# Kernel tuning notes

Hardware: AMD Instinct MI355X
Metric: run time of the kernel (lower is better)

## Reference

```python
import jax, jax.numpy as jnp
import numpy as np

D_MODEL, D_STATE, D_CONV, EXPAND = 1024, 16, 4, 2
D_INNER = EXPAND * D_MODEL          # 2048
DT_RANK = D_MODEL // 16             # 64
B, L = 2, 1024


def setup_inputs() -> dict:
    key = jax.random.key(0)
    ks = jax.random.split(key, 10)
    x = jax.random.normal(ks[0], (B, L, D_MODEL), dtype=jnp.float32)
    ln_w = jnp.ones((D_MODEL,), jnp.float32)
    ln_b = jnp.zeros((D_MODEL,), jnp.float32)
    in_proj_w = jax.random.normal(ks[1], (2 * D_INNER, D_MODEL), jnp.float32) * (D_MODEL ** -0.5)
    conv_w = jax.random.normal(ks[2], (D_INNER, 1, D_CONV), jnp.float32) * (D_CONV ** -0.5)
    conv_b = jnp.zeros((D_INNER,), jnp.float32)
    x_proj_w = jax.random.normal(ks[3], (DT_RANK + 2 * D_STATE, D_INNER), jnp.float32) * (D_INNER ** -0.5)
    dt_proj_w = jax.random.normal(ks[4], (D_INNER, DT_RANK), jnp.float32) * (DT_RANK ** -0.5)
    # dt bias: inverse-softplus of dt sampled log-uniform in [1e-3, 1e-1] (mamba init)
    dt = jnp.exp(jax.random.uniform(ks[5], (D_INNER,)) * (np.log(0.1) - np.log(1e-3)) + np.log(1e-3))
    dt_proj_b = dt + jnp.log(-jnp.expm1(-dt))
    # A_log: log of [1..d_state] repeated per channel (S4D-real init)
    A_log = jnp.log(jnp.broadcast_to(jnp.arange(1, D_STATE + 1, dtype=jnp.float32), (D_INNER, D_STATE)))
    D = jnp.ones((D_INNER,), jnp.float32)
    out_proj_w = jax.random.normal(ks[6], (D_MODEL, D_INNER), jnp.float32) * (D_INNER ** -0.5)
    return dict(x=x, ln_w=ln_w, ln_b=ln_b, in_proj_w=in_proj_w, conv_w=conv_w,
                conv_b=conv_b, x_proj_w=x_proj_w, dt_proj_w=dt_proj_w,
                dt_proj_b=dt_proj_b, A_log=A_log, D=D, out_proj_w=out_proj_w)


def _layernorm(x, w, b, eps=1e-5):
    mu = jnp.mean(x, axis=-1, keepdims=True)
    var = jnp.mean(jnp.square(x - mu), axis=-1, keepdims=True)
    return (x - mu) * jax.lax.rsqrt(var + eps) * w + b


def _mamba(h, in_proj_w, conv_w, conv_b, x_proj_w, dt_proj_w, dt_proj_b, A_log, D, out_proj_w):
    # h: (B, L, d_model)
    xz = jnp.einsum('bld,ed->ble', h, in_proj_w)          # (B,L,2*d_inner)
    x_in, z = jnp.split(xz, 2, axis=-1)                   # each (B,L,d_inner)
    # depthwise causal conv1d
    kernel = jnp.transpose(conv_w, (2, 1, 0))             # (d_conv, 1, d_inner) LIO
    x_conv = jax.lax.conv_general_dilated(
        x_in, kernel, window_strides=(1,), padding=[(D_CONV - 1, 0)],
        dimension_numbers=('NLC', 'LIO', 'NLC'), feature_group_count=D_INNER)
    x_conv = jax.nn.silu(x_conv + conv_b)                 # (B,L,d_inner)
    # input-dependent SSM parameters
    x_dbl = jnp.einsum('bld,ed->ble', x_conv, x_proj_w)   # (B,L,dt_rank+2*d_state)
    dt, B_ssm, C_ssm = jnp.split(x_dbl, [DT_RANK, DT_RANK + D_STATE], axis=-1)
    dt = jax.nn.softplus(jnp.einsum('blr,dr->bld', dt, dt_proj_w) + dt_proj_b)  # (B,L,d_inner)
    A = -jnp.exp(A_log)                                   # (d_inner, d_state)
    deltaA = jnp.exp(dt[..., None] * A)                   # (B,L,d_inner,d_state)
    deltaBu = dt[..., None] * B_ssm[:, :, None, :] * x_conv[..., None]
    # selective scan: h_t = deltaA_t * h_{t-1} + deltaBu_t (parallel associative scan over L)
    def combine(left, right):
        a_l, b_l = left
        a_r, b_r = right
        return a_l * a_r, b_l * a_r + b_r
    _, states = jax.lax.associative_scan(combine, (deltaA, deltaBu), axis=1)
    y = jnp.einsum('blds,bls->bld', states, C_ssm) + x_conv * D
    y = y * jax.nn.silu(z)
    return jnp.einsum('bld,ed->ble', y, out_proj_w)       # (B,L,d_model)


def reference(x, ln_w, ln_b, in_proj_w, conv_w, conv_b, x_proj_w, dt_proj_w,
              dt_proj_b, A_log, D, out_proj_w):
    h = _layernorm(x, ln_w, ln_b)
    return x + _mamba(h, in_proj_w, conv_w, conv_b, x_proj_w, dt_proj_w,
                      dt_proj_b, A_log, D, out_proj_w)
```

## Files before the change

kernel.cpp:

```cpp
#include <hip/hip_runtime.h>
#include <hip/hip_bf16.h>
#include <math.h>

#define DM   1024
#define DI   2048
#define DS   16
#define DTR  64
#define NB   2
#define LL   1024
#define MR   (NB*LL)
#define XDBL 96
#define NC   32
#define CL   32

typedef _Float16 half8  __attribute__((ext_vector_type(8)));
typedef _Float16 half4v __attribute__((ext_vector_type(4)));
typedef float    floatx4 __attribute__((ext_vector_type(4)));

__device__ __forceinline__ void gload_lds16(const void* g, void* l) {
  __builtin_amdgcn_global_load_lds(
      (const __attribute__((address_space(1))) void*)g,
      (__attribute__((address_space(3))) void*)l, 16, 0, 0);
}

__global__ __launch_bounds__(256) void front_kernel(
    const float* __restrict__ x, const float* __restrict__ ln_w,
    const float* __restrict__ ln_b,
    const float* __restrict__ w_in, const float* __restrict__ w_out,
    const float* __restrict__ w_xp, const float* __restrict__ w_dt,
    _Float16* __restrict__ h_h,
    _Float16* __restrict__ w_in_h, _Float16* __restrict__ w_out_h,
    _Float16* __restrict__ w_xp_h, _Float16* __restrict__ w_dt_h) {
  const int blk = blockIdx.x;
  if (blk < MR) {
    __shared__ float sA[4], sB[4];
    const float* xr = x + (size_t)blk * DM;
    float s = 0.f, ss = 0.f;
    for (int i = threadIdx.x; i < DM; i += 256) {
      float v = xr[i];
      s += v; ss += v * v;
    }
    for (int o = 32; o > 0; o >>= 1) {
      s  += __shfl_down(s, o, 64);
      ss += __shfl_down(ss, o, 64);
    }
    const int wid = threadIdx.x >> 6, lid = threadIdx.x & 63;
    if (lid == 0) { sA[wid] = s; sB[wid] = ss; }
    __syncthreads();
    if (threadIdx.x == 0) {
      float S = sA[0] + sA[1] + sA[2] + sA[3];
      float SS = sB[0] + sB[1] + sB[2] + sB[3];
      float mu = S / DM;
      sA[0] = mu;
      sB[0] = rsqrtf(SS / DM - mu * mu + 1e-5f);
    }
    __syncthreads();
    const float mu = sA[0], rs = sB[0];
    for (int i = threadIdx.x; i < DM; i += 256)
      h_h[(size_t)blk * DM + i] = (_Float16)((xr[i] - mu) * rs * ln_w[i] + ln_b[i]);
    return;
  }
  int i = (blk - MR) * 256 + threadIdx.x;
  const int N0 = 1048576, N1 = 524288, N2 = 49152, N3 = 32768;
  const float* s; _Float16* d; int off;
  if (i < N0)            { s = w_in;  d = w_in_h;  off = i; }
  else if (i < N0+N1)    { s = w_out; d = w_out_h; off = i - N0; }
  else if (i < N0+N1+N2) { s = w_xp;  d = w_xp_h;  off = i - N0 - N1; }
  else if (i < N0+N1+N2+N3) { s = w_dt; d = w_dt_h; off = i - N0 - N1 - N2; }
  else return;
  float4 v = ((const float4*)s)[off];
  half4v h = {(_Float16)v.x, (_Float16)v.y, (_Float16)v.z, (_Float16)v.w};
  ((half4v*)d)[off] = h;
}

template <int EPI, int TN>
__global__ __launch_bounds__(256) void gemm_mfma(
    const _Float16* __restrict__ A,
    const _Float16* __restrict__ W,
    void* __restrict__ Cv, void* __restrict__ C2v,
    const float* __restrict__ extra, int ldc,
    int M, int N, int K, int kchunk) {
  constexpr int NT = (TN + 31) / 32;
  constexpr int WSLOT = TN / 16;
  constexpr int LPS = 2 + (WSLOT >= 8 ? 2 : 1);
  __shared__ alignas(16) _Float16 As[4][128 * 32];
  __shared__ alignas(16) _Float16 Ws[4][TN * 32];
  const int t = threadIdx.x;
  const int wave = t >> 6, lane = t & 63;
  const int m0 = blockIdx.y * 128, n0 = blockIdx.x * TN;
  const int k_beg = blockIdx.z * kchunk;
  const int nk = kchunk / 32;
  const int wm = (wave >> 1) * 64, wn = (wave & 1) * (TN / 2);
  floatx4 acc[4][NT];
#pragma unroll
  for (int i = 0; i < 4; i++)
#pragma unroll
    for (int j = 0; j < NT; j++) acc[i][j] = {0.f, 0.f, 0.f, 0.f};

  const int fr = lane & 15;
  const int kc8 = lane >> 4;
  const int kp = (kc8 ^ ((fr >> 1) & 3)) * 8;

  auto stage = [&](int buf, int k0) {
    for (int sl = wave; sl < 8; sl += 4) {
      const int idx = sl * 64 + lane;
      const int row = idx >> 2;
      const int kc = (idx & 3) ^ ((row >> 1) & 3);
      gload_lds16(A + (size_t)(m0 + row) * K + k0 + kc * 8,
                  &As[buf][sl * 512]);
    }
    for (int sl = wave; sl < WSLOT; sl += 4) {
      const int idx = sl * 64 + lane;
      const int row = idx >> 2;
      const int kc = (idx & 3) ^ ((row >> 1) & 3);
      const int wrow = (n0 + row < N) ? row : 0;
      gload_lds16(W + (size_t)(n0 + wrow) * K + k0 + kc * 8,
                  &Ws[buf][sl * 512]);
    }
  };

  const int npre = nk < 3 ? nk : 3;
  for (int p = 0; p < npre; p++) stage(p, k_beg + p * 32);

  for (int ki = 0; ki < nk; ki++) {
    const int rem = nk - 1 - ki;
    if (rem >= 2)
      asm volatile("s_waitcnt vmcnt(%0)" :: "n"(2 * LPS) : "memory");
    else if (rem == 1)
      asm volatile("s_waitcnt vmcnt(%0)" :: "n"(LPS) : "memory");
    else
      asm volatile("s_waitcnt vmcnt(0)" ::: "memory");
    __builtin_amdgcn_s_barrier();
    const int cur = ki & 3;
    half8 af[4], wf[NT];
#pragma unroll
    for (int i = 0; i < 4; i++)
      af[i] = *(const half8*)&As[cur][(wm + i * 16 + fr) * 32 + kp];
#pragma unroll
    for (int j = 0; j < NT; j++)
      wf[j] = *(const half8*)&Ws[cur][(wn + j * 16 + fr) * 32 + kp];
    __builtin_amdgcn_s_setprio(1);
#pragma unroll
    for (int i = 0; i < 4; i++)
#pragma unroll
      for (int j = 0; j < NT; j++)
        acc[i][j] = __builtin_amdgcn_mfma_f32_16x16x32_f16(af[i], wf[j], acc[i][j], 0, 0, 0);
    __builtin_amdgcn_s_setprio(0);
    if (ki + 3 < nk) stage((ki + 3) & 3, k_beg + (ki + 3) * 32);
  }

  const int col = lane & 15, rowq = lane >> 4;
#pragma unroll
  for (int i = 0; i < 4; i++) {
#pragma unroll
    for (int j = 0; j < NT; j++) {
      const int n = n0 + wn + j * 16 + col;
      if (n < N) {
#pragma unroll
        for (int r = 0; r < 4; r++) {
          const int m = m0 + wm + i * 16 + rowq * 4 + r;
          float v = acc[i][j][r];
          if (EPI == 0) {
            if (n < DI) ((_Float16*)Cv )[(size_t)m * DI + n]      = (_Float16)v;
            else        ((_Float16*)C2v)[(size_t)m * DI + n - DI] = (_Float16)v;
          } else if (EPI == 4) {
            ((_Float16*)Cv)[((size_t)blockIdx.z * M + m) * ldc + n] = (_Float16)v;
          } else if (EPI == 5) {
            v += extra[n];
            v = (v > 20.f) ? v : __logf(1.f + __expf(v));
            ((_Float16*)Cv)[(size_t)m * ldc + n] = (_Float16)v;
          }
        }
      }
    }
  }
}

__global__ __launch_bounds__(256) void xproj_reduce(
    const _Float16* __restrict__ part,
    float* __restrict__ x_dbl, _Float16* __restrict__ dtr) {
  const int idx = blockIdx.x * 256 + threadIdx.x;
  const int m = idx / XDBL, c = idx - m * XDBL;
  float s = 0.f;
#pragma unroll
  for (int z = 0; z < 16; z++) s += (float)part[(size_t)z * (MR * XDBL) + idx];
  x_dbl[idx] = s;
  if (c < DTR) dtr[m * DTR + c] = (_Float16)s;
}

__global__ __launch_bounds__(256) void out_reduce(
    const float* __restrict__ x, const _Float16* __restrict__ part,
    float* __restrict__ out) {
  const int i = blockIdx.x * 256 + threadIdx.x;
  float4 a = ((const float4*)x)[i];
#pragma unroll
  for (int z = 0; z < 4; z++) {
    half4v p = ((const half4v*)(part + (size_t)z * MR * DM))[i];
    a.x += (float)p.x; a.y += (float)p.y; a.z += (float)p.z; a.w += (float)p.w;
  }
  ((float4*)out)[i] = a;
}

__global__ __launch_bounds__(256) void conv_silu_kernel(
    const _Float16* __restrict__ xin, const float* __restrict__ cw,
    const float* __restrict__ cb, _Float16* __restrict__ xc) {
  const int idx = blockIdx.x * 256 + threadIdx.x;
  const int d8 = idx & (DI / 8 - 1);
  const int ml = idx >> 8;
  const int l  = ml & (LL - 1);
  const int d0 = d8 * 8;
  half8 xr[4];
  const half8 zero = {0, 0, 0, 0, 0, 0, 0, 0};
#pragma unroll
  for (int k = 0; k < 4; k++) {
    const int lp = l - 3 + k;
    xr[k] = (lp >= 0) ? *(const half8*)&xin[(size_t)(ml - 3 + k) * DI + d0] : zero;
  }
  half8 o;
#pragma unroll
  for (int j = 0; j < 8; j++) {
    float acc = cb[d0 + j];
#pragma unroll
    for (int k = 0; k < 4; k++)
      acc += (float)xr[k][j] * cw[(d0 + j) * 4 + k];
    o[j] = (_Float16)(acc / (1.f + __expf(-acc)));
  }
  *(half8*)&xc[(size_t)ml * DI + d0] = o;
}

__device__ __forceinline__ bool load_a(const float* __restrict__ A_log, int d,
                                       float* a) {
  const float4* Ap = (const float4*)(A_log + (size_t)d * DS);
  bool fast = true;
#pragma unroll
  for (int i = 0; i < 4; i++) {
    float4 v = Ap[i];
    a[4 * i + 0] = -__expf(v.x); a[4 * i + 1] = -__expf(v.y);
    a[4 * i + 2] = -__expf(v.z); a[4 * i + 3] = -__expf(v.w);
  }
#pragma unroll
  for (int s = 0; s < DS; s++)
    fast = fast && (fabsf(a[s] + (float)(s + 1)) < 1e-4f);
  return fast;
}

__global__ __launch_bounds__(256) void scan_phase1(
    const _Float16* __restrict__ xc,
    const float* __restrict__ xdbl,
    const _Float16* __restrict__ dtm,
    const float* __restrict__ A_log,
    float* __restrict__ HE,
    float* __restrict__ SA) {
  __shared__ float Bs[CL][DS];
  const int bi = blockIdx.x;
  const int dblk = bi & 7;
  const int c = (bi >> 3) & (NC - 1);
  const int b = bi >> 8;
  const int t = threadIdx.x;
  const int d = dblk * 256 + t;
  const int mlbase = b * LL + c * CL;

  for (int i = t; i < CL * DS; i += 256) {
    int tt = i >> 4, s = i & 15;
    Bs[tt][s] = xdbl[(size_t)(mlbase + tt) * XDBL + DTR + s];
  }

  float a[DS];
  const bool fast = load_a(A_log, d, a);
  float h[DS];
#pragma unroll
  for (int s = 0; s < DS; s++) h[s] = 0.f;
  float S = 0.f;
  __syncthreads();

  if (fast) {
    for (int tt = 0; tt < CL; tt++) {
      const size_t ml = mlbase + tt;
      const float dtv = (float)dtm[ml * DI + d];
      const float u   = (float)xc[ml * DI + d];
      const float du  = dtv * u;
      S += dtv;
      const float r = __expf(-dtv);
      float P = 1.f;
#pragma unroll
      for (int s = 0; s < DS; s++) {
        P *= r;
        h[s] = P * h[s] + du * Bs[tt][s];
      }
    }
  } else {
    for (int tt = 0; tt < CL; tt++) {
      const size_t ml = mlbase + tt;
      const float dtv = (float)dtm[ml * DI + d];
      const float u   = (float)xc[ml * DI + d];
      const float du  = dtv * u;
      S += dtv;
#pragma unroll
      for (int s = 0; s < DS; s++)
        h[s] = __expf(dtv * a[s]) * h[s] + du * Bs[tt][s];
    }
  }
  const size_t base = ((size_t)(b * NC + c) * DS) * DI + d;
#pragma unroll
  for (int s = 0; s < DS; s++) HE[base + (size_t)s * DI] = h[s];
  SA[(size_t)(b * NC + c) * DI + d] = S;
}

__global__ __launch_bounds__(256) void scan_phase2(
    const float* __restrict__ A_log,
    const float* __restrict__ SA,
    float* __restrict__ HE) {
  const int idx = blockIdx.x * 256 + threadIdx.x;
  const int d = idx & (DI - 1);
  const int s = (idx >> 11) & (DS - 1);
  const int b = idx >> 15;
  const float a = -__expf(A_log[(size_t)d * DS + s]);
  float Hc = 0.f;
  for (int c = 0; c < NC; c++) {
    const size_t o = ((size_t)(b * NC + c) * DS + s) * DI + d;
    const float he = HE[o];
    const float P = __expf(a * SA[(size_t)(b * NC + c) * DI + d]);
    HE[o] = Hc;
    Hc = P * Hc + he;
  }
}

__global__ __launch_bounds__(256) void scan_phase3(
    const _Float16* __restrict__ xc,
    const float* __restrict__ xdbl,
    const _Float16* __restrict__ dtm,
    const _Float16* __restrict__ zbuf,
    const float* __restrict__ A_log,
    const float* __restrict__ Dvec,
    const float* __restrict__ HE,
    _Float16* __restrict__ y) {
  __shared__ float Bs[CL][DS];
  __shared__ float Cs[CL][DS];
  const int bi = blockIdx.x;
  const int dblk = bi & 7;
  const int c = (bi >> 3) & (NC - 1);
  const int b = bi >> 8;
  const int t = threadIdx.x;
  const int d = dblk * 256 + t;
  const int mlbase = b * LL + c * CL;

  for (int i = t; i < CL * DS; i += 256) {
    int tt = i >> 4, s = i & 15;
    const size_t ro = (size_t)(mlbase + tt) * XDBL + DTR + s;
    Bs[tt][s] = xdbl[ro];
    Cs[tt][s] = xdbl[ro + DS];
  }

  float a[DS];
  const bool fast = load_a(A_log, d, a);
  float h[DS];
  const size_t base = ((size_t)(b * NC + c) * DS) * DI + d;
#pragma unroll
  for (int s = 0; s < DS; s++) h[s] = HE[base + (size_t)s * DI];
  const float Dv = Dvec[d];
  __syncthreads();

  if (fast) {
    for (int tt = 0; tt < CL; tt++) {
      const size_t ml = mlbase + tt;
      const float dtv = (float)dtm[ml * DI + d];
      const float u   = (float)xc[ml * DI + d];
      const float du  = dtv * u;
      const float r = __expf(-dtv);
      float P = 1.f, p = 0.f;
#pragma unroll
      for (int s = 0; s < DS; s++) {
        P *= r;
        h[s] = P * h[s] + du * Bs[tt][s];
        p += h[s] * Cs[tt][s];
      }
      const float zv = (float)zbuf[ml * DI + d];
      const float sil = zv / (1.f + __expf(-zv));
      y[ml * DI + d] = (_Float16)((p + u * Dv) * sil);
    }
  } else {
    for (int tt = 0; tt < CL; tt++) {
      const size_t ml = mlbase + tt;
      const float dtv = (float)dtm[ml * DI + d];
      const float u   = (float)xc[ml * DI + d];
      const float du  = dtv * u;
      float p = 0.f;
#pragma unroll
      for (int s = 0; s < DS; s++) {
        h[s] = __expf(dtv * a[s]) * h[s] + du * Bs[tt][s];
        p += h[s] * Cs[tt][s];
      }
      const float zv = (float)zbuf[ml * DI + d];
      const float sil = zv / (1.f + __expf(-zv));
      y[ml * DI + d] = (_Float16)((p + u * Dv) * sil);
    }
  }
}

extern "C" void kernel_launch(void* const* d_in, const int* in_sizes, int n_in,
                              void* d_out, int out_size, void* d_ws, size_t ws_size,
                              hipStream_t stream) {
  const float* x         = (const float*)d_in[0];
  const float* ln_w      = (const float*)d_in[1];
  const float* ln_b      = (const float*)d_in[2];
  const float* in_proj_w = (const float*)d_in[3];
  const float* conv_w    = (const float*)d_in[4];
  const float* conv_b    = (const float*)d_in[5];
  const float* x_proj_w  = (const float*)d_in[6];
  const float* dt_proj_w = (const float*)d_in[7];
  const float* dt_proj_b = (const float*)d_in[8];
  const float* A_log     = (const float*)d_in[9];
  const float* Dvec      = (const float*)d_in[10];
  const float* out_proj_w= (const float*)d_in[11];
  float* out = (float*)d_out;

  char* ws = (char*)d_ws;
  _Float16* h_h      = (_Float16*)ws;
  _Float16* xin_h    = (_Float16*)(ws + 4194304);
  _Float16* y_h      = xin_h;
  _Float16* z_h      = (_Float16*)(ws + 12582912);
  _Float16* xc_h     = (_Float16*)(ws + 20971520);
  _Float16* dtb_h    = (_Float16*)(ws + 29360128);
  _Float16* out_part = dtb_h;
  float*    x_dbl    = (float*)   (ws + 46137344);
  float*    SA       = (float*)   (ws + 46923776);
  _Float16* dtr_h    = (_Float16*)(ws + 47448064);
  float*    HE       = (float*)   (ws + 47710208);
  _Float16* w_in_h   = (_Float16*)(ws + 56098816);
  _Float16* w_out_h  = (_Float16*)(ws + 64487424);
  _Float16* w_xp_h   = (_Float16*)(ws + 68681728);
  _Float16* w_dt_h   = (_Float16*)(ws + 69074944);
  _Float16* xp_part  = (_Float16*)(ws + 69337088);

  front_kernel<<<MR + 6464, 256, 0, stream>>>(
      x, ln_w, ln_b, in_proj_w, out_proj_w, x_proj_w, dt_proj_w,
      h_h, w_in_h, w_out_h, w_xp_h, w_dt_h);

  gemm_mfma<0, 128><<<dim3(2 * DI / 128, MR / 128, 1), 256, 0, stream>>>(
      h_h, w_in_h, xin_h, z_h, nullptr, 0, MR, 2 * DI, DM, DM);

  conv_silu_kernel<<<(MR * DI / 8) / 256, 256, 0, stream>>>(xin_h, conv_w, conv_b, xc_h);

  gemm_mfma<4, 96><<<dim3(1, MR / 128, 16), 256, 0, stream>>>(
      xc_h, w_xp_h, xp_part, nullptr, nullptr, XDBL, MR, XDBL, DI, DI / 16);
  xproj_reduce<<<(MR * XDBL) / 256, 256, 0, stream>>>(xp_part, x_dbl, dtr_h);

  gemm_mfma<5, 64><<<dim3(DI / 64, MR / 128, 1), 256, 0, stream>>>(
      dtr_h, w_dt_h, dtb_h, nullptr, dt_proj_b, DI, MR, DI, DTR, DTR);

  scan_phase1<<<NB * NC * (DI / 256), 256, 0, stream>>>(
      xc_h, x_dbl, dtb_h, A_log, HE, SA);
  scan_phase2<<<(NB * DS * DI) / 256, 256, 0, stream>>>(A_log, SA, HE);
  scan_phase3<<<NB * NC * (DI / 256), 256, 0, stream>>>(
      xc_h, x_dbl, dtb_h, z_h, A_log, Dvec, HE, y_h);

  gemm_mfma<4, 128><<<dim3(DM / 128, MR / 128, 4), 256, 0, stream>>>(
      y_h, w_out_h, out_part, nullptr, nullptr, DM, MR, DM, DI, DI / 4);
  out_reduce<<<(MR * DM / 4) / 256, 256, 0, stream>>>(x, out_part, out);
}
```

Measured before the change: 224.8 us.

## Replace split-K partial buffers with atomic accumulation and fuse dt projection input conversion

The x_proj and out_proj split-K GEMMs now accumulate straight into fp32 outputs with atomicAdd. This removes the xproj_reduce and out_reduce kernels and their partial buffers. The residual is seeded by having the layernorm kernel copy x into out, and x_dbl is zeroed inside the conv kernel. A dedicated dt_kernel converts x_dbl to fp16 on the fly and applies bias plus softplus. Scan chunking also changes from 32 chunks of 32 to 16 chunks of 64. Atomics add contention and make the summation order nondeterministic.

```diff
diff --git a/kernel.cpp b/kernel.cpp
--- a/kernel.cpp
+++ b/kernel.cpp
@@ -10,8 +10,8 @@
 #define LL   1024
 #define MR   (NB*LL)
 #define XDBL 96
-#define NC   32
-#define CL   32
+#define NC   16
+#define CL   64
 
 typedef _Float16 half8  __attribute__((ext_vector_type(8)));
 typedef _Float16 half4v __attribute__((ext_vector_type(4)));
@@ -28,7 +28,7 @@
     const float* __restrict__ ln_b,
     const float* __restrict__ w_in, const float* __restrict__ w_out,
     const float* __restrict__ w_xp, const float* __restrict__ w_dt,
-    _Float16* __restrict__ h_h,
+    _Float16* __restrict__ h_h, float* __restrict__ out,
     _Float16* __restrict__ w_in_h, _Float16* __restrict__ w_out_h,
     _Float16* __restrict__ w_xp_h, _Float16* __restrict__ w_dt_h) {
   const int blk = blockIdx.x;
@@ -56,8 +56,11 @@
     }
     __syncthreads();
     const float mu = sA[0], rs = sB[0];
-    for (int i = threadIdx.x; i < DM; i += 256)
-      h_h[(size_t)blk * DM + i] = (_Float16)((xr[i] - mu) * rs * ln_w[i] + ln_b[i]);
+    for (int i = threadIdx.x; i < DM; i += 256) {
+      const float v = xr[i];
+      out[(size_t)blk * DM + i] = v;
+      h_h[(size_t)blk * DM + i] = (_Float16)((v - mu) * rs * ln_w[i] + ln_b[i]);
+    }
     return;
   }
   int i = (blk - MR) * 256 + threadIdx.x;
@@ -77,14 +80,13 @@
 __global__ __launch_bounds__(256) void gemm_mfma(
     const _Float16* __restrict__ A,
     const _Float16* __restrict__ W,
-    void* __restrict__ Cv, void* __restrict__ C2v,
-    const float* __restrict__ extra, int ldc,
+    void* __restrict__ Cv, void* __restrict__ C2v, int ldc,
     int M, int N, int K, int kchunk) {
   constexpr int NT = (TN + 31) / 32;
   constexpr int WSLOT = TN / 16;
   constexpr int LPS = 2 + (WSLOT >= 8 ? 2 : 1);
-  __shared__ alignas(16) _Float16 As[4][128 * 32];
-  __shared__ alignas(16) _Float16 Ws[4][TN * 32];
+  __shared__ alignas(16) _Float16 As[4][4096];
+  __shared__ alignas(16) _Float16 Ws[4][4096];
   const int t = threadIdx.x;
   const int wave = t >> 6, lane = t & 63;
   const int m0 = blockIdx.y * 128, n0 = blockIdx.x * TN;
@@ -106,16 +108,14 @@
       const int idx = sl * 64 + lane;
       const int row = idx >> 2;
       const int kc = (idx & 3) ^ ((row >> 1) & 3);
-      gload_lds16(A + (size_t)(m0 + row) * K + k0 + kc * 8,
-                  &As[buf][sl * 512]);
+      gload_lds16(A + (size_t)(m0 + row) * K + k0 + kc * 8, &As[buf][sl * 512]);
     }
     for (int sl = wave; sl < WSLOT; sl += 4) {
       const int idx = sl * 64 + lane;
       const int row = idx >> 2;
       const int kc = (idx & 3) ^ ((row >> 1) & 3);
       const int wrow = (n0 + row < N) ? row : 0;
-      gload_lds16(W + (size_t)(n0 + wrow) * K + k0 + kc * 8,
-                  &Ws[buf][sl * 512]);
+      gload_lds16(W + (size_t)(n0 + wrow) * K + k0 + kc * 8, &Ws[buf][sl * 512]);
     }
   };
 
@@ -163,12 +163,8 @@
           if (EPI == 0) {
             if (n < DI) ((_Float16*)Cv )[(size_t)m * DI + n]      = (_Float16)v;
             else        ((_Float16*)C2v)[(size_t)m * DI + n - DI] = (_Float16)v;
-          } else if (EPI == 4) {
-            ((_Float16*)Cv)[((size_t)blockIdx.z * M + m) * ldc + n] = (_Float16)v;
-          } else if (EPI == 5) {
-            v += extra[n];
-            v = (v > 20.f) ? v : __logf(1.f + __expf(v));
-            ((_Float16*)Cv)[(size_t)m * ldc + n] = (_Float16)v;
+          } else if (EPI == 6) {
+            atomicAdd(&((float*)Cv)[(size_t)m * ldc + n], v);
           }
         }
       }
@@ -176,35 +172,81 @@
   }
 }
 
-__global__ __launch_bounds__(256) void xproj_reduce(
-    const _Float16* __restrict__ part,
-    float* __restrict__ x_dbl, _Float16* __restrict__ dtr) {
-  const int idx = blockIdx.x * 256 + threadIdx.x;
-  const int m = idx / XDBL, c = idx - m * XDBL;
-  float s = 0.f;
-#pragma unroll
-  for (int z = 0; z < 16; z++) s += (float)part[(size_t)z * (MR * XDBL) + idx];
-  x_dbl[idx] = s;
-  if (c < DTR) dtr[m * DTR + c] = (_Float16)s;
-}
-
-__global__ __launch_bounds__(256) void out_reduce(
-    const float* __restrict__ x, const _Float16* __restrict__ part,
-    float* __restrict__ out) {
-  const int i = blockIdx.x * 256 + threadIdx.x;
-  float4 a = ((const float4*)x)[i];
-#pragma unroll
-  for (int z = 0; z < 4; z++) {
-    half4v p = ((const half4v*)(part + (size_t)z * MR * DM))[i];
-    a.x += (float)p.x; a.y += (float)p.y; a.z += (float)p.z; a.w += (float)p.w;
-  }
-  ((float4*)out)[i] = a;
+__global__ __launch_bounds__(256) void dt_kernel(
+    const float* __restrict__ xdbl, const _Float16* __restrict__ W,
+    const float* __restrict__ bias, _Float16* __restrict__ dtb) {
+  __shared__ alignas(16) _Float16 As[2][4096];
+  __shared__ alignas(16) _Float16 Ws[2][2048];
+  const int t = threadIdx.x, wave = t >> 6, lane = t & 63;
+  const int m0 = blockIdx.y * 128, n0 = blockIdx.x * 64;
+  for (int q = wave; q < 16; q += 4) {
+    const int ss = q >> 3, sl = q & 7;
+    const int idx = sl * 64 + lane;
+    const int row = idx >> 2;
+    const int kc = (idx & 3) ^ ((row >> 1) & 3);
+    const float* src = xdbl + (size_t)(m0 + row) * XDBL + ss * 32 + kc * 8;
+    float4 a = ((const float4*)src)[0];
+    float4 b = ((const float4*)src)[1];
+    half8 h = {(_Float16)a.x, (_Float16)a.y, (_Float16)a.z, (_Float16)a.w,
+               (_Float16)b.x, (_Float16)b.y, (_Float16)b.z, (_Float16)b.w};
+    *(half8*)&As[ss][sl * 512 + lane * 8] = h;
+  }
+  for (int q = wave; q < 8; q += 4) {
+    const int ss = q >> 2, sw = q & 3;
+    const int idx = sw * 64 + lane;
+    const int row = idx >> 2;
+    const int kc = (idx & 3) ^ ((row >> 1) & 3);
+    gload_lds16(W + (size_t)(n0 + row) * DTR + ss * 32 + kc * 8,
+                &Ws[ss][sw * 512]);
+  }
+  asm volatile("s_waitcnt vmcnt(0)" ::: "memory");
+  __syncthreads();
+  const int fr = lane & 15, kc8 = lane >> 4;
+  const int kp = (kc8 ^ ((fr >> 1) & 3)) * 8;
+  const int wm = (wave >> 1) * 64, wn = (wave & 1) * 32;
+  floatx4 acc[4][2];
+#pragma unroll
+  for (int i = 0; i < 4; i++)
+#pragma unroll
+    for (int j = 0; j < 2; j++) acc[i][j] = {0.f, 0.f, 0.f, 0.f};
+#pragma unroll
+  for (int ss = 0; ss < 2; ss++) {
+    half8 af[4], wf[2];
+#pragma unroll
+    for (int i = 0; i < 4; i++)
+      af[i] = *(const half8*)&As[ss][(wm + i * 16 + fr) * 32 + kp];
+#pragma unroll
+    for (int j = 0; j < 2; j++)
+      wf[j] = *(const half8*)&Ws[ss][(wn + j * 16 + fr) * 32 + kp];
+#pragma unroll
+    for (int i = 0; i < 4; i++)
+#pragma unroll
+      for (int j = 0; j < 2; j++)
+        acc[i][j] = __builtin_amdgcn_mfma_f32_16x16x32_f16(af[i], wf[j], acc[i][j], 0, 0, 0);
+  }
+  const int col = lane & 15, rowq = lane >> 4;
+#pragma unroll
+  for (int i = 0; i < 4; i++) {
+#pragma unroll
+    for (int j = 0; j < 2; j++) {
+      const int n = n0 + wn + j * 16 + col;
+#pragma unroll
+      for (int r = 0; r < 4; r++) {
+        const int m = m0 + wm + i * 16 + rowq * 4 + r;
+        float v = acc[i][j][r] + bias[n];
+        v = (v > 20.f) ? v : __logf(1.f + __expf(v));
+        dtb[(size_t)m * DI + n] = (_Float16)v;
+      }
+    }
+  }
 }
 
 __global__ __launch_bounds__(256) void conv_silu_kernel(
     const _Float16* __restrict__ xin, const float* __restrict__ cw,
-    const float* __restrict__ cb, _Float16* __restrict__ xc) {
+    const float* __restrict__ cb, _Float16* __restrict__ xc,
+    float* __restrict__ xdbl) {
   const int idx = blockIdx.x * 256 + threadIdx.x;
+  if (idx < MR * XDBL) xdbl[idx] = 0.f;
   const int d8 = idx & (DI / 8 - 1);
   const int ml = idx >> 8;
   const int l  = ml & (LL - 1);
@@ -255,7 +297,7 @@
   const int bi = blockIdx.x;
   const int dblk = bi & 7;
   const int c = (bi >> 3) & (NC - 1);
-  const int b = bi >> 8;
+  const int b = bi >> 7;
   const int t = threadIdx.x;
   const int d = dblk * 256 + t;
   const int mlbase = b * LL + c * CL;
@@ -339,7 +381,7 @@
   const int bi = blockIdx.x;
   const int dblk = bi & 7;
   const int c = (bi >> 3) & (NC - 1);
-  const int b = bi >> 8;
+  const int b = bi >> 7;
   const int t = threadIdx.x;
   const int d = dblk * 256 + t;
   const int mlbase = b * LL + c * CL;
@@ -421,32 +463,29 @@
   _Float16* z_h      = (_Float16*)(ws + 12582912);
   _Float16* xc_h     = (_Float16*)(ws + 20971520);
   _Float16* dtb_h    = (_Float16*)(ws + 29360128);
-  _Float16* out_part = dtb_h;
   float*    x_dbl    = (float*)   (ws + 46137344);
   float*    SA       = (float*)   (ws + 46923776);
-  _Float16* dtr_h    = (_Float16*)(ws + 47448064);
   float*    HE       = (float*)   (ws + 47710208);
   _Float16* w_in_h   = (_Float16*)(ws + 56098816);
   _Float16* w_out_h  = (_Float16*)(ws + 64487424);
   _Float16* w_xp_h   = (_Float16*)(ws + 68681728);
   _Float16* w_dt_h   = (_Float16*)(ws + 69074944);
-  _Float16* xp_part  = (_Float16*)(ws + 69337088);
 
   front_kernel<<<MR + 6464, 256, 0, stream>>>(
       x, ln_w, ln_b, in_proj_w, out_proj_w, x_proj_w, dt_proj_w,
-      h_h, w_in_h, w_out_h, w_xp_h, w_dt_h);
+      h_h, out, w_in_h, w_out_h, w_xp_h, w_dt_h);
 
   gemm_mfma<0, 128><<<dim3(2 * DI / 128, MR / 128, 1), 256, 0, stream>>>(
-      h_h, w_in_h, xin_h, z_h, nullptr, 0, MR, 2 * DI, DM, DM);
-
-  conv_silu_kernel<<<(MR * DI / 8) / 256, 256, 0, stream>>>(xin_h, conv_w, conv_b, xc_h);
-
-  gemm_mfma<4, 96><<<dim3(1, MR / 128, 16), 256, 0, stream>>>(
-      xc_h, w_xp_h, xp_part, nullptr, nullptr, XDBL, MR, XDBL, DI, DI / 16);
-  xproj_reduce<<<(MR * XDBL) / 256, 256, 0, stream>>>(xp_part, x_dbl, dtr_h);
-
-  gemm_mfma<5, 64><<<dim3(DI / 64, MR / 128, 1), 256, 0, stream>>>(
-      dtr_h, w_dt_h, dtb_h, nullptr, dt_proj_b, DI, MR, DI, DTR, DTR);
+      h_h, w_in_h, xin_h, z_h, 0, MR, 2 * DI, DM, DM);
+
+  conv_silu_kernel<<<(MR * DI / 8) / 256, 256, 0, stream>>>(
+      xin_h, conv_w, conv_b, xc_h, x_dbl);
+
+  gemm_mfma<6, 96><<<dim3(1, MR / 128, 32), 256, 0, stream>>>(
+      xc_h, w_xp_h, x_dbl, nullptr, XDBL, MR, XDBL, DI, DI / 32);
+
+  dt_kernel<<<dim3(DI / 64, MR / 128), 256, 0, stream>>>(
+      x_dbl, w_dt_h, dt_proj_b, dtb_h);
 
   scan_phase1<<<NB * NC * (DI / 256), 256, 0, stream>>>(
       xc_h, x_dbl, dtb_h, A_log, HE, SA);
@@ -454,7 +493,6 @@
   scan_phase3<<<NB * NC * (DI / 256), 256, 0, stream>>>(
       xc_h, x_dbl, dtb_h, z_h, A_log, Dvec, HE, y_h);
 
-  gemm_mfma<4, 128><<<dim3(DM / 128, MR / 128, 4), 256, 0, stream>>>(
-      y_h, w_out_h, out_part, nullptr, nullptr, DM, MR, DM, DI, DI / 4);
-  out_reduce<<<(MR * DM / 4) / 256, 256, 0, stream>>>(x, out_part, out);
-}
+  gemm_mfma<6, 128><<<dim3(DM / 128, MR / 128, 4), 256, 0, stream>>>(
+      y_h, w_out_h, out, nullptr, DM, MR, DM, DI, DI / 4);
+}
```

After: 265.1 us. 1.18x slower.

## Fuse causal conv+SiLU into x_proj GEMM and precompute A table in front kernel

Applied to the files above, without the earlier changes.

The separate depthwise conv+SiLU kernel is removed. A new xproj_conv kernel computes conv+SiLU for its 128x128 tile, writes it straight into LDS as the GEMM A operand, and also stores xc to global for the scan. The front kernel gains extra blocks that precompute -exp(A_log) and a per-channel flag for the fast path, so the scan kernels load a table instead of recomputing exps. This saves one launch and one full read of xc before the x_proj GEMM. The trade-off is a single-shot GEMM with no load pipelining and conv work duplicated across the K-split grid layout.

```diff
diff --git a/kernel.cpp b/kernel.cpp
--- a/kernel.cpp
+++ b/kernel.cpp
@@ -28,9 +28,11 @@
     const float* __restrict__ ln_b,
     const float* __restrict__ w_in, const float* __restrict__ w_out,
     const float* __restrict__ w_xp, const float* __restrict__ w_dt,
+    const float* __restrict__ A_log,
     _Float16* __restrict__ h_h,
     _Float16* __restrict__ w_in_h, _Float16* __restrict__ w_out_h,
-    _Float16* __restrict__ w_xp_h, _Float16* __restrict__ w_dt_h) {
+    _Float16* __restrict__ w_xp_h, _Float16* __restrict__ w_dt_h,
+    float* __restrict__ atab, unsigned char* __restrict__ aflag) {
   const int blk = blockIdx.x;
   if (blk < MR) {
     __shared__ float sA[4], sB[4];
@@ -58,6 +60,20 @@
     const float mu = sA[0], rs = sB[0];
     for (int i = threadIdx.x; i < DM; i += 256)
       h_h[(size_t)blk * DM + i] = (_Float16)((xr[i] - mu) * rs * ln_w[i] + ln_b[i]);
+    return;
+  }
+  if (blk >= MR + 6464) {
+    const int d = (blk - (MR + 6464)) * 256 + threadIdx.x;
+    if (d < DI) {
+      bool fast = true;
+#pragma unroll
+      for (int s = 0; s < DS; s++) {
+        const float a = -__expf(A_log[(size_t)d * DS + s]);
+        atab[(size_t)d * DS + s] = a;
+        fast = fast && (fabsf(a + (float)(s + 1)) < 1e-4f);
+      }
+      aflag[d] = fast ? 1 : 0;
+    }
     return;
   }
   int i = (blk - MR) * 256 + threadIdx.x;
@@ -83,8 +99,8 @@
   constexpr int NT = (TN + 31) / 32;
   constexpr int WSLOT = TN / 16;
   constexpr int LPS = 2 + (WSLOT >= 8 ? 2 : 1);
-  __shared__ alignas(16) _Float16 As[4][128 * 32];
-  __shared__ alignas(16) _Float16 Ws[4][TN * 32];
+  __shared__ alignas(16) _Float16 As[4][4096];
+  __shared__ alignas(16) _Float16 Ws[4][4096];
   const int t = threadIdx.x;
   const int wave = t >> 6, lane = t & 63;
   const int m0 = blockIdx.y * 128, n0 = blockIdx.x * TN;
@@ -106,16 +122,14 @@
       const int idx = sl * 64 + lane;
       const int row = idx >> 2;
       const int kc = (idx & 3) ^ ((row >> 1) & 3);
-      gload_lds16(A + (size_t)(m0 + row) * K + k0 + kc * 8,
-                  &As[buf][sl * 512]);
+      gload_lds16(A + (size_t)(m0 + row) * K + k0 + kc * 8, &As[buf][sl * 512]);
     }
     for (int sl = wave; sl < WSLOT; sl += 4) {
       const int idx = sl * 64 + lane;
       const int row = idx >> 2;
       const int kc = (idx & 3) ^ ((row >> 1) & 3);
       const int wrow = (n0 + row < N) ? row : 0;
-      gload_lds16(W + (size_t)(n0 + wrow) * K + k0 + kc * 8,
-                  &Ws[buf][sl * 512]);
+      gload_lds16(W + (size_t)(n0 + wrow) * K + k0 + kc * 8, &Ws[buf][sl * 512]);
     }
   };
 
@@ -176,6 +190,89 @@
   }
 }
 
+__global__ __launch_bounds__(256) void xproj_conv(
+    const _Float16* __restrict__ xin, const _Float16* __restrict__ W,
+    const float* __restrict__ cw, const float* __restrict__ cb,
+    _Float16* __restrict__ part, _Float16* __restrict__ xc) {
+  __shared__ alignas(16) _Float16 As[4][4096];
+  __shared__ alignas(16) _Float16 Ws[4][3072];
+  const int t = threadIdx.x, wave = t >> 6, lane = t & 63;
+  const int m0 = blockIdx.y * 128;
+  const int k0 = blockIdx.z * 128;
+  for (int q = t; q < 2048; q += 256) {
+    const int ss = q >> 9, idx = q & 511;
+    const int row = idx >> 2;
+    const int kc = (idx & 3) ^ ((row >> 1) & 3);
+    const int m = m0 + row;
+    const int l = m & (LL - 1);
+    const int dbase = k0 + ss * 32 + kc * 8;
+    float accv[8];
+#pragma unroll
+    for (int j = 0; j < 8; j++) accv[j] = cb[dbase + j];
+#pragma unroll
+    for (int k = 0; k < 4; k++) {
+      const int lp = l - 3 + k;
+      if (lp >= 0) {
+        half8 xv = *(const half8*)&xin[(size_t)(m - 3 + k) * DI + dbase];
+#pragma unroll
+        for (int j = 0; j < 8; j++)
+          accv[j] += (float)xv[j] * cw[(dbase + j) * 4 + k];
+      }
+    }
+    half8 o;
+#pragma unroll
+    for (int j = 0; j < 8; j++)
+      o[j] = (_Float16)(accv[j] / (1.f + __expf(-accv[j])));
+    *(half8*)&As[ss][idx * 8] = o;
+    *(half8*)&xc[(size_t)m * DI + dbase] = o;
+  }
+  for (int q = wave; q < 24; q += 4) {
+    const int ss = q / 6, sw = q % 6;
+    const int idx = sw * 64 + lane;
+    const int row = idx >> 2;
+    const int kc = (idx & 3) ^ ((row >> 1) & 3);
+    gload_lds16(W + (size_t)row * DI + k0 + ss * 32 + kc * 8, &Ws[ss][sw * 512]);
+  }
+  asm volatile("s_waitcnt vmcnt(0)" ::: "memory");
+  __syncthreads();
+  const int fr = lane & 15, kc8 = lane >> 4;
+  const int kp = (kc8 ^ ((fr >> 1) & 3)) * 8;
+  const int wm = (wave >> 1) * 64, wn = (wave & 1) * 48;
+  floatx4 acc[4][3];
+#pragma unroll
+  for (int i = 0; i < 4; i++)
+#pragma unroll
+    for (int j = 0; j < 3; j++) acc[i][j] = {0.f, 0.f, 0.f, 0.f};
+#pragma unroll
+  for (int ss = 0; ss < 4; ss++) {
+    half8 af[4], wf[3];
+#pragma unroll
+    for (int i = 0; i < 4; i++)
+      af[i] = *(const half8*)&As[ss][(wm + i * 16 + fr) * 32 + kp];
+#pragma unroll
+    for (int j = 0; j < 3; j++)
+      wf[j] = *(const half8*)&Ws[ss][(wn + j * 16 + fr) * 32 + kp];
+#pragma unroll
+    for (int i = 0; i < 4; i++)
+#pragma unroll
+      for (int j = 0; j < 3; j++)
+        acc[i][j] = __builtin_amdgcn_mfma_f32_16x16x32_f16(af[i], wf[j], acc[i][j], 0, 0, 0);
+  }
+  const int col = lane & 15, rowq = lane >> 4;
+#pragma unroll
+  for (int i = 0; i < 4; i++) {
+#pragma unroll
+    for (int j = 0; j < 3; j++) {
+      const int n = wn + j * 16 + col;
+#pragma unroll
+      for (int r = 0; r < 4; r++) {
+        const int m = m0 + wm + i * 16 + rowq * 4 + r;
+        part[((size_t)blockIdx.z * MR + m) * XDBL + n] = (_Float16)acc[i][j][r];
+      }
+    }
+  }
+}
+
 __global__ __launch_bounds__(256) void xproj_reduce(
     const _Float16* __restrict__ part,
     float* __restrict__ x_dbl, _Float16* __restrict__ dtr) {
@@ -201,56 +298,11 @@
   ((float4*)out)[i] = a;
 }
 
-__global__ __launch_bounds__(256) void conv_silu_kernel(
-    const _Float16* __restrict__ xin, const float* __restrict__ cw,
-    const float* __restrict__ cb, _Float16* __restrict__ xc) {
-  const int idx = blockIdx.x * 256 + threadIdx.x;
-  const int d8 = idx & (DI / 8 - 1);
-  const int ml = idx >> 8;
-  const int l  = ml & (LL - 1);
-  const int d0 = d8 * 8;
-  half8 xr[4];
-  const half8 zero = {0, 0, 0, 0, 0, 0, 0, 0};
-#pragma unroll
-  for (int k = 0; k < 4; k++) {
-    const int lp = l - 3 + k;
-    xr[k] = (lp >= 0) ? *(const half8*)&xin[(size_t)(ml - 3 + k) * DI + d0] : zero;
-  }
-  half8 o;
-#pragma unroll
-  for (int j = 0; j < 8; j++) {
-    float acc = cb[d0 + j];
-#pragma unroll
-    for (int k = 0; k < 4; k++)
-      acc += (float)xr[k][j] * cw[(d0 + j) * 4 + k];
-    o[j] = (_Float16)(acc / (1.f + __expf(-acc)));
-  }
-  *(half8*)&xc[(size_t)ml * DI + d0] = o;
-}
-
-__device__ __forceinline__ bool load_a(const float* __restrict__ A_log, int d,
-                                       float* a) {
-  const float4* Ap = (const float4*)(A_log + (size_t)d * DS);
-  bool fast = true;
-#pragma unroll
-  for (int i = 0; i < 4; i++) {
-    float4 v = Ap[i];
-    a[4 * i + 0] = -__expf(v.x); a[4 * i + 1] = -__expf(v.y);
-    a[4 * i + 2] = -__expf(v.z); a[4 * i + 3] = -__expf(v.w);
-  }
-#pragma unroll
-  for (int s = 0; s < DS; s++)
-    fast = fast && (fabsf(a[s] + (float)(s + 1)) < 1e-4f);
-  return fast;
-}
-
 __global__ __launch_bounds__(256) void scan_phase1(
-    const _Float16* __restrict__ xc,
-    const float* __restrict__ xdbl,
+    const _Float16* __restrict__ xc, const float* __restrict__ xdbl,
     const _Float16* __restrict__ dtm,
-    const float* __restrict__ A_log,
-    float* __restrict__ HE,
-    float* __restrict__ SA) {
+    const float* __restrict__ atab, const unsigned char* __restrict__ aflag,
+    float* __restrict__ HE, float* __restrict__ SA) {
   __shared__ float Bs[CL][DS];
   const int bi = blockIdx.x;
   const int dblk = bi & 7;
@@ -265,8 +317,12 @@
     Bs[tt][s] = xdbl[(size_t)(mlbase + tt) * XDBL + DTR + s];
   }
 
+  const bool fast = aflag[d] != 0;
   float a[DS];
-  const bool fast = load_a(A_log, d, a);
+  if (!fast) {
+#pragma unroll
+    for (int s = 0; s < DS; s++) a[s] = atab[(size_t)d * DS + s];
+  }
   float h[DS];
 #pragma unroll
   for (int s = 0; s < DS; s++) h[s] = 0.f;
@@ -307,14 +363,14 @@
 }
 
 __global__ __launch_bounds__(256) void scan_phase2(
-    const float* __restrict__ A_log,
+    const float* __restrict__ atab,
     const float* __restrict__ SA,
     float* __restrict__ HE) {
   const int idx = blockIdx.x * 256 + threadIdx.x;
   const int d = idx & (DI - 1);
   const int s = (idx >> 11) & (DS - 1);
   const int b = idx >> 15;
-  const float a = -__expf(A_log[(size_t)d * DS + s]);
+  const float a = atab[(size_t)d * DS + s];
   float Hc = 0.f;
   for (int c = 0; c < NC; c++) {
     const size_t o = ((size_t)(b * NC + c) * DS + s) * DI + d;
@@ -326,13 +382,10 @@
 }
 
 __global__ __launch_bounds__(256) void scan_phase3(
-    const _Float16* __restrict__ xc,
-    const float* __restrict__ xdbl,
-    const _Float16* __restrict__ dtm,
-    const _Float16* __restrict__ zbuf,
-    const float* __restrict__ A_log,
-    const float* __restrict__ Dvec,
-    const float* __restrict__ HE,
+    const _Float16* __restrict__ xc, const float* __restrict__ xdbl,
+    const _Float16* __restrict__ dtm, const _Float16* __restrict__ zbuf,
+    const float* __restrict__ atab, const unsigned char* __restrict__ aflag,
+    const float* __restrict__ Dvec, const float* __restrict__ HE,
     _Float16* __restrict__ y) {
   __shared__ float Bs[CL][DS];
   __shared__ float Cs[CL][DS];
@@ -351,8 +404,12 @@
     Cs[tt][s] = xdbl[ro + DS];
   }
 
+  const bool fast = aflag[d] != 0;
   float a[DS];
-  const bool fast = load_a(A_log, d, a);
+  if (!fast) {
+#pragma unroll
+    for (int s = 0; s < DS; s++) a[s] = atab[(size_t)d * DS + s];
+  }
   float h[DS];
   const size_t base = ((size_t)(b * NC + c) * DS) * DI + d;
 #pragma unroll
@@ -422,6 +479,8 @@
   _Float16* xc_h     = (_Float16*)(ws + 20971520);
   _Float16* dtb_h    = (_Float16*)(ws + 29360128);
   _Float16* out_part = dtb_h;
+  float*    atab     = (float*)   (ws + 37748736);
+  unsigned char* aflag = (unsigned char*)(ws + 37879808);
   float*    x_dbl    = (float*)   (ws + 46137344);
   float*    SA       = (float*)   (ws + 46923776);
   _Float16* dtr_h    = (_Float16*)(ws + 47448064);
@@ -432,29 +491,29 @@
   _Float16* w_dt_h   = (_Float16*)(ws + 69074944);
   _Float16* xp_part  = (_Float16*)(ws + 69337088);
 
-  front_kernel<<<MR + 6464, 256, 0, stream>>>(
-      x, ln_w, ln_b, in_proj_w, out_proj_w, x_proj_w, dt_proj_w,
-      h_h, w_in_h, w_out_h, w_xp_h, w_dt_h);
+  front_kernel<<<MR + 6464 + 8, 256, 0, stream>>>(
+      x, ln_w, ln_b, in_proj_w, out_proj_w, x_proj_w, dt_proj_w, A_log,
+      h_h, w_in_h, w_out_h, w_xp_h, w_dt_h, atab, aflag);
 
   gemm_mfma<0, 128><<<dim3(2 * DI / 128, MR / 128, 1), 256, 0, stream>>>(
       h_h, w_in_h, xin_h, z_h, nullptr, 0, MR, 2 * DI, DM, DM);
 
-  conv_silu_kernel<<<(MR * DI / 8) / 256, 256, 0, stream>>>(xin_h, conv_w, conv_b, xc_h);
-
-  gemm_mfma<4, 96><<<dim3(1, MR / 128, 16), 256, 0, stream>>>(
-      xc_h, w_xp_h, xp_part, nullptr, nullptr, XDBL, MR, XDBL, DI, DI / 16);
+  xproj_conv<<<dim3(1, MR / 128, 16), 256, 0, stream>>>(
+      xin_h, w_xp_h, conv_w, conv_b, xp_part, xc_h);
+
   xproj_reduce<<<(MR * XDBL) / 256, 256, 0, stream>>>(xp_part, x_dbl, dtr_h);
 
   gemm_mfma<5, 64><<<dim3(DI / 64, MR / 128, 1), 256, 0, stream>>>(
       dtr_h, w_dt_h, dtb_h, nullptr, dt_proj_b, DI, MR, DI, DTR, DTR);
 
   scan_phase1<<<NB * NC * (DI / 256), 256, 0, stream>>>(
-      xc_h, x_dbl, dtb_h, A_log, HE, SA);
-  scan_phase2<<<(NB * DS * DI) / 256, 256, 0, stream>>>(A_log, SA, HE);
+      xc_h, x_dbl, dtb_h, atab, aflag, HE, SA);
+  scan_phase2<<<(NB * DS * DI) / 256, 256, 0, stream>>>(atab, SA, HE);
   scan_phase3<<<NB * NC * (DI / 256), 256, 0, stream>>>(
-      xc_h, x_dbl, dtb_h, z_h, A_log, Dvec, HE, y_h);
+      xc_h, x_dbl, dtb_h, z_h, atab, aflag, Dvec, HE, y_h);
 
   gemm_mfma<4, 128><<<dim3(DM / 128, MR / 128, 4), 256, 0, stream>>>(
       y_h, w_out_h, out_part, nullptr, nullptr, DM, MR, DM, DI, DI / 4);
+
   out_reduce<<<(MR * DM / 4) / 256, 256, 0, stream>>>(x, out_part, out);
 }
```

New measurement: 228.0 us. About the same (+1.4%).
